# Kernel optimization log

Hardware: AMD Instinct MI355X
Metric: run time of the kernel (lower is better)

## Reference

```python
import jax, jax.numpy as jnp
import numpy as np

L, B, D, H = 2048, 2, 1024, 16
HD = D // H
NEG_INF = float('-inf')


def setup_inputs() -> dict:
    key = jax.random.key(0)
    ks = jax.random.split(key, 12)
    query = jax.random.normal(ks[0], (L, B, D), jnp.float32)
    key_t = jax.random.normal(ks[1], (L, B, D), jnp.float32)
    value = jax.random.normal(ks[2], (L, B, D), jnp.float32)
    # causal attention mask (True = masked)
    attn_mask = jnp.triu(jnp.ones((L, L), dtype=bool), k=1)
    # pad last 128 source positions of batch element 1
    key_pad_mask = jnp.zeros((B, L), dtype=bool).at[1, L - 128:].set(True)
    s = 1.0 / np.sqrt(D)
    Wq = jax.random.normal(ks[3], (D, D), jnp.float32) * s
    bq = jnp.zeros((D,), jnp.float32)
    Wk = jax.random.normal(ks[4], (D, D), jnp.float32) * s
    bk = jnp.zeros((D,), jnp.float32)
    Wv = jax.random.normal(ks[5], (D, D), jnp.float32) * s
    bv = jnp.zeros((D,), jnp.float32)
    Wo = jax.random.normal(ks[6], (D, D), jnp.float32) * s
    bo = jnp.zeros((D,), jnp.float32)
    return {"query": query, "key": key_t, "value": value,
            "key_pad_mask": key_pad_mask, "attn_mask": attn_mask,
            "Wq": Wq, "bq": bq, "Wk": Wk, "bk": bk,
            "Wv": Wv, "bv": bv, "Wo": Wo, "bo": bo}


def reference(query, key, value, key_pad_mask, attn_mask,
              Wq, bq, Wk, bk, Wv, bv, Wo, bo):
    # projections: torch Linear is x @ W.T + b
    q = query @ Wq.T + bq          # (L, B, D)
    k = key @ Wk.T + bk            # (L, B, D)
    v = value @ Wv.T + bv          # (L, B, D)
    # split heads: (L, B, D) -> (B, H, L, hd)
    def split(x):
        return x.reshape(L, B, H, HD).transpose(1, 2, 0, 3)
    q, k, v = split(q), split(k), split(v)
    # NOTE: source module never applies scale_factor (bug kept for fidelity)
    scores = jnp.einsum('bhld,bhsd->bhls', q, k)  # (B, H, L, L)
    scores = jnp.where(attn_mask[None, None, :, :], NEG_INF, scores)
    scores = jnp.where(key_pad_mask[:, None, None, :], NEG_INF, scores)
    attn = jax.nn.softmax(scores, axis=-1)
    # dropout is identity in eval mode
    out = jnp.einsum('bhls,bhsd->bhld', attn, v)  # (B, H, L, hd)
    out = out.transpose(2, 0, 1, 3).reshape(L, B, D)
    return out @ Wo.T + bo
```

## Files before the change

kernel.cpp:

```cpp
#include <hip/hip_runtime.h>
#include <hip/hip_bf16.h>

#define LL 2048
#define BB 2
#define DD 1024
#define HH 16
#define HDIM 64
#define MM (LL*BB)
#define PADROW 30

typedef _Float16 f16x8 __attribute__((ext_vector_type(8)));
typedef _Float16 f16x4 __attribute__((ext_vector_type(4)));
typedef float   f32x4  __attribute__((ext_vector_type(4)));
typedef float   f32x16 __attribute__((ext_vector_type(16)));
typedef unsigned int u32x4 __attribute__((ext_vector_type(4)));

__device__ __forceinline__ void gload16(const void* g, void* l) {
  __builtin_amdgcn_global_load_lds(
      (const __attribute__((address_space(1))) void*)g,
      (__attribute__((address_space(3))) void*)l,
      16, 0, 0);
}

__device__ __forceinline__ unsigned int pkrtz(float a, float b) {
  auto r = __builtin_amdgcn_cvt_pkrtz(a, b);
  return __builtin_bit_cast(unsigned int, r);
}

__global__ __launch_bounds__(256) void cvt_f32_f16(
    const float* __restrict__ q, const float* __restrict__ k, const float* __restrict__ v,
    const float* __restrict__ wq, const float* __restrict__ wk,
    const float* __restrict__ wv, const float* __restrict__ wo,
    _Float16* __restrict__ xq, _Float16* __restrict__ xk, _Float16* __restrict__ xv,
    _Float16* __restrict__ whq, _Float16* __restrict__ whk,
    _Float16* __restrict__ whv, _Float16* __restrict__ who)
{
  const float* s; _Float16* d; int n;
  switch (blockIdx.y) {
    case 0: s = q;  d = xq;  n = MM*DD;  break;
    case 1: s = k;  d = xk;  n = MM*DD;  break;
    case 2: s = v;  d = xv;  n = MM*DD;  break;
    case 3: s = wq; d = whq; n = DD*DD;  break;
    case 4: s = wk; d = whk; n = DD*DD;  break;
    case 5: s = wv; d = whv; n = DD*DD;  break;
    default: s = wo; d = who; n = DD*DD; break;
  }
  int i = (blockIdx.x * 256 + threadIdx.x) * 8;
  if (i >= n) return;
  float4 a = *reinterpret_cast<const float4*>(s + i);
  float4 b = *reinterpret_cast<const float4*>(s + i + 4);
  f16x8 h;
  h[0] = (_Float16)a.x; h[1] = (_Float16)a.y; h[2] = (_Float16)a.z; h[3] = (_Float16)a.w;
  h[4] = (_Float16)b.x; h[5] = (_Float16)b.y; h[6] = (_Float16)b.z; h[7] = (_Float16)b.w;
  *reinterpret_cast<f16x8*>(d + i) = h;
}

__global__ __launch_bounds__(256) void gemm_nt(
    const _Float16* __restrict__ X0, const _Float16* __restrict__ X1, const _Float16* __restrict__ X2,
    const _Float16* __restrict__ W0, const _Float16* __restrict__ W1, const _Float16* __restrict__ W2,
    const float* __restrict__ B0, const float* __restrict__ B1, const float* __restrict__ B2,
    _Float16* __restrict__ dq, _Float16* __restrict__ dk, _Float16* __restrict__ dvt,
    float* __restrict__ dof, int mode_base)
{
  const int K = DD;
  __shared__ alignas(16) _Float16 Ah[128][64];
  __shared__ alignas(16) _Float16 Bh[128][64];
  int z = blockIdx.z;
  const _Float16* X = (z == 0) ? X0 : ((z == 1) ? X1 : X2);
  const _Float16* W = (z == 0) ? W0 : ((z == 1) ? W1 : W2);
  const float* bias = (z == 0) ? B0 : ((z == 1) ? B1 : B2);
  int mode = mode_base + z;
  int tid = threadIdx.x, w = tid >> 6, lane = tid & 63;
  int bb = blockIdx.x;
  int mt = ((bb & 7) * 4 + ((bb >> 3) & 3)) * 128;
  int nt = (bb >> 5) * 128;

  f32x4 acc[4][4];
  #pragma unroll
  for (int i = 0; i < 4; ++i)
    #pragma unroll
    for (int j = 0; j < 4; ++j) acc[i][j] = (f32x4){0.f, 0.f, 0.f, 0.f};

  for (int kt = 0; kt < K; kt += 64) {
    __syncthreads();
    #pragma unroll
    for (int i = 0; i < 4; ++i) {
      int r0 = w * 32 + i * 8;
      int row = r0 + (lane >> 3);
      gload16(X + (size_t)(mt + row) * K + kt + (lane & 7) * 8, &Ah[r0][0]);
      gload16(W + (size_t)(nt + row) * K + kt + (lane & 7) * 8, &Bh[r0][0]);
    }
    __syncthreads();
    #pragma unroll
    for (int kk = 0; kk < 2; ++kk) {
      f16x8 af[4], bf[4];
      #pragma unroll
      for (int f = 0; f < 4; ++f) {
        af[f] = *(const f16x8*)&Ah[(w >> 1) * 64 + f * 16 + (lane & 15)][kk * 32 + (lane >> 4) * 8];
        bf[f] = *(const f16x8*)&Bh[(w & 1) * 64 + f * 16 + (lane & 15)][kk * 32 + (lane >> 4) * 8];
      }
      #pragma unroll
      for (int fm = 0; fm < 4; ++fm)
        #pragma unroll
        for (int fn = 0; fn < 4; ++fn)
          acc[fm][fn] = __builtin_amdgcn_mfma_f32_16x16x32_f16(af[fm], bf[fn], acc[fm][fn], 0, 0, 0);
    }
  }

  #pragma unroll
  for (int fm = 0; fm < 4; ++fm) {
    #pragma unroll
    for (int fn = 0; fn < 4; ++fn) {
      #pragma unroll
      for (int j = 0; j < 4; ++j) {
        int m = mt + (w >> 1) * 64 + fm * 16 + (lane >> 4) * 4 + j;
        int n = nt + (w & 1) * 64 + fn * 16 + (lane & 15);
        float val = acc[fm][fn][j] + bias[n];
        if (mode == 3) {
          dof[(size_t)m * DD + n] = val;
        } else {
          int lseq = m >> 1, bb2 = m & 1;
          int h = n >> 6, hd = n & 63;
          int bh = bb2 * HH + h;
          int s = hd >> 4, hi2 = (hd >> 3) & 1, ii = hd & 7;
          if (mode == 0) {
            int g = lseq >> 5, lo2 = lseq & 31;
            size_t idx = ((((size_t)(bh * 64 + g)) * 4 + s) * 64 + (hi2 * 32 + lo2)) * 8 + ii;
            dq[idx] = (_Float16)val;
          } else if (mode == 1) {
            int t = lseq >> 6, u = (lseq >> 5) & 1, lo2 = lseq & 31;
            size_t idx = ((((size_t)(bh * 32 + t)) * 8 + (u * 4 + s)) * 64 + (hi2 * 32 + lo2)) * 8 + ii;
            dk[idx] = (_Float16)val;
          } else {
            int t = lseq >> 6, rem = lseq & 63;
            int ks = rem >> 4, hiv = (rem >> 3) & 1, iv = rem & 7;
            int vv = hd >> 5, lov = hd & 31;
            size_t idx = ((((size_t)(bh * 32 + t)) * 8 + (vv * 4 + ks)) * 64 + (hiv * 32 + lov)) * 8 + iv;
            dvt[idx] = (_Float16)val;
          }
        }
      }
    }
  }
}

__global__ __launch_bounds__(64, 2) void attn_partial(
    const _Float16* __restrict__ q_ws,
    const _Float16* __restrict__ k_ws,
    const _Float16* __restrict__ vt_ws,
    _Float16* __restrict__ po,
    float* __restrict__ pm,
    float* __restrict__ pl)
{
  int lane = threadIdx.x;
  int lo = lane & 31, hi = lane >> 5;

  int lin = blockIdx.x;
  int k8 = lin & 7, m2 = lin >> 3;
  int half = m2 & 1;
  int bh = k8 * 4 + ((m2 >> 1) & 3);
  int g = 63 - (m2 >> 3);
  int b = bh >> 4;

  const int td = g >> 1;
  int np = td + 1;
  if (b == 1 && np > PADROW) np = PADROW;
  int h1 = (np + 1) >> 1;
  int c0 = half ? h1 : 0;
  int c1 = half ? np : h1;

  int qab = g * 32 + lo;

  f32x16 o0, o1;
  #pragma unroll
  for (int r = 0; r < 16; ++r) { o0[r] = 0.f; o1[r] = 0.f; }
  float m_run = -1e30f, l_run = 0.f;

  if (c0 < c1) {
    const _Float16* qb = q_ws + ((size_t)(bh * 64 + g)) * 2048 + lane * 8;
    f16x8 qf[4];
    #pragma unroll
    for (int s = 0; s < 4; ++s) qf[s] = *(const f16x8*)(qb + s * 512);

    auto loadK = [&](int t, f16x8 (&kf)[8]) __attribute__((always_inline)) {
      const _Float16* kg = k_ws + ((size_t)(bh * 32 + t)) * 4096 + lane * 8;
      #pragma unroll
      for (int f = 0; f < 8; ++f)
        kf[f] = *(const f16x8*)(kg + f * 512);
    };

    auto body = [&](int t, const f16x8 (&kf)[8]) __attribute__((always_inline)) {
      f16x8 vf[8];
      const _Float16* vg = vt_ws + ((size_t)(bh * 32 + t)) * 4096 + lane * 8;
      #pragma unroll
      for (int f = 0; f < 8; ++f)
        vf[f] = *(const f16x8*)(vg + f * 512);

      f32x16 s0, s1;
      #pragma unroll
      for (int r = 0; r < 16; ++r) { s0[r] = 0.f; s1[r] = 0.f; }
      #pragma unroll
      for (int s = 0; s < 4; ++s) {
        s0 = __builtin_amdgcn_mfma_f32_32x32x16_f16(kf[s],     qf[s], s0, 0, 0, 0);
        s1 = __builtin_amdgcn_mfma_f32_32x32x16_f16(kf[4 + s], qf[s], s1, 0, 0, 0);
      }

      if (t == td) {
        #pragma unroll
        for (int r = 0; r < 16; ++r) {
          int kv0 = t * 64 + (r & 3) + 8 * (r >> 2) + 4 * hi;
          if (kv0 > qab)      s0[r] = -1e30f;
          if (kv0 + 32 > qab) s1[r] = -1e30f;
        }
      }

      float pmax = -1e30f;
      #pragma unroll
      for (int r = 0; r < 16; ++r) pmax = fmaxf(pmax, fmaxf(s0[r], s1[r]));
      pmax = fmaxf(pmax, __shfl_xor(pmax, 32));
      float mn = fmaxf(m_run, pmax);
      float sc = __expf(m_run - mn);
      m_run = mn;
      float rs = 0.f;
      #pragma unroll
      for (int r = 0; r < 16; ++r) {
        s0[r] = __expf(s0[r] - mn); rs += s0[r];
        s1[r] = __expf(s1[r] - mn); rs += s1[r];
      }
      rs += __shfl_xor(rs, 32);
      l_run = l_run * sc + rs;
      #pragma unroll
      for (int r = 0; r < 16; ++r) { o0[r] *= sc; o1[r] *= sc; }

      unsigned int W0[8], W1[8];
      #pragma unroll
      for (int wi = 0; wi < 8; ++wi) {
        int r0 = (wi >> 1) * 4 + (wi & 1) * 2;
        W0[wi] = pkrtz(s0[r0], s0[r0 + 1]);
        W1[wi] = pkrtz(s1[r0], s1[r0 + 1]);
      }

      #define DO_KS(W, KS, VA, VB)                                            \
      {                                                                       \
        const int q4 = ((KS) & 1) * 4;                                        \
        unsigned int sA = hi ? W[q4 + 0] : W[q4 + 2];                         \
        unsigned int sB = hi ? W[q4 + 1] : W[q4 + 3];                         \
        unsigned int rA = (unsigned int)__shfl_xor((int)sA, 32);              \
        unsigned int rB = (unsigned int)__shfl_xor((int)sB, 32);              \
        unsigned int own0 = hi ? W[q4 + 2] : W[q4 + 0];                       \
        unsigned int own1 = hi ? W[q4 + 3] : W[q4 + 1];                       \
        u32x4 wv;                                                             \
        wv[0] = hi ? rA : own0;  wv[1] = hi ? rB : own1;                      \
        wv[2] = hi ? own0 : rA;  wv[3] = hi ? own1 : rB;                      \
        f16x8 PB = __builtin_bit_cast(f16x8, wv);                             \
        o0 = __builtin_amdgcn_mfma_f32_32x32x16_f16(VA, PB, o0, 0, 0, 0);     \
        o1 = __builtin_amdgcn_mfma_f32_32x32x16_f16(VB, PB, o1, 0, 0, 0);     \
      }
      DO_KS(W0, 0, vf[0], vf[4])
      DO_KS(W0, 1, vf[1], vf[5])
      DO_KS(W1, 2, vf[2], vf[6])
      DO_KS(W1, 3, vf[3], vf[7])
      #undef DO_KS
    };

    f16x8 kfA[8], kfB[8];
    int t = c0;
    loadK(t, kfA);
    while (true) {
      if (t + 1 < c1) loadK(t + 1, kfB);
      body(t, kfA);
      if (++t >= c1) break;
      if (t + 1 < c1) loadK(t + 1, kfA);
      body(t, kfB);
      if (++t >= c1) break;
    }
  }

  size_t pidx = ((size_t)(bh * 64 + g) << 1) | half;
  _Float16* pb = po + pidx * 2048 + (size_t)lo * 64;
  #pragma unroll
  for (int rq = 0; rq < 4; ++rq) {
    f16x4 a, c;
    #pragma unroll
    for (int j = 0; j < 4; ++j) {
      a[j] = (_Float16)o0[rq * 4 + j];
      c[j] = (_Float16)o1[rq * 4 + j];
    }
    *(f16x4*)(pb + rq * 8 + hi * 4)      = a;
    *(f16x4*)(pb + 32 + rq * 8 + hi * 4) = c;
  }
  if (hi == 0) {
    pm[pidx * 32 + lo] = m_run;
    pl[pidx * 32 + lo] = l_run;
  }
}

__global__ __launch_bounds__(256) void attn_merge(
    const _Float16* __restrict__ po, const float* __restrict__ pm,
    const float* __restrict__ pl, _Float16* __restrict__ ao)
{
  int tid = threadIdx.x;
  int rowl = tid >> 3, dseg = tid & 7;
  int grow = blockIdx.x * 32 + rowl;
  int bh = grow >> 11;
  int rem = grow & 2047;
  int g = rem >> 5;
  int rr = rem & 31;
  size_t pidxA = ((size_t)(bh * 64 + g)) << 1;
  size_t pidxB = pidxA | 1;
  float mA = pm[pidxA * 32 + rr], mB = pm[pidxB * 32 + rr];
  float lA = pl[pidxA * 32 + rr], lB = pl[pidxB * 32 + rr];
  float mx = fmaxf(mA, mB);
  float fA = __expf(mA - mx), fB = __expf(mB - mx);
  float inv = 1.0f / (lA * fA + lB * fB);
  f16x8 a = *(const f16x8*)&po[pidxA * 2048 + rr * 64 + dseg * 8];
  f16x8 bvv = *(const f16x8*)&po[pidxB * 2048 + rr * 64 + dseg * 8];
  f16x8 outv;
  #pragma unroll
  for (int i = 0; i < 8; ++i)
    outv[i] = (_Float16)((((float)a[i]) * fA + ((float)bvv[i]) * fB) * inv);
  int b = bh >> 4, h = bh & 15;
  *(f16x8*)&ao[((size_t)rem * BB + b) * DD + h * 64 + dseg * 8] = outv;
}

extern "C" void kernel_launch(void* const* d_in, const int* in_sizes, int n_in,
                              void* d_out, int out_size, void* d_ws, size_t ws_size,
                              hipStream_t stream) {
  const float* q  = (const float*)d_in[0];
  const float* k  = (const float*)d_in[1];
  const float* v  = (const float*)d_in[2];
  const float* Wq = (const float*)d_in[5];
  const float* bq = (const float*)d_in[6];
  const float* Wk = (const float*)d_in[7];
  const float* bk = (const float*)d_in[8];
  const float* Wv = (const float*)d_in[9];
  const float* bv = (const float*)d_in[10];
  const float* Wo = (const float*)d_in[11];
  const float* bo = (const float*)d_in[12];
  float* out = (float*)d_out;

  _Float16* ws = (_Float16*)d_ws;
  const size_t MD = (size_t)MM * DD;
  const size_t WD = (size_t)DD * DD;
  _Float16* xq   = ws;
  _Float16* xk   = xq + MD;
  _Float16* xv   = xk + MD;
  _Float16* whq  = xv + MD;
  _Float16* whk  = whq + WD;
  _Float16* whv  = whk + WD;
  _Float16* who  = whv + WD;
  _Float16* qws  = who + WD;
  _Float16* kws  = qws + MD;
  _Float16* vtws = kws + MD;
  _Float16* aows = vtws + MD;

  _Float16* po = ws;
  float* pm = (float*)(ws + 3 * MD);
  float* pl = pm + 4096 * 32;

  cvt_f32_f16<<<dim3(2048, 7), 256, 0, stream>>>(
      q, k, v, Wq, Wk, Wv, Wo, xq, xk, xv, whq, whk, whv, who);

  gemm_nt<<<dim3(256, 1, 3), 256, 0, stream>>>(
      xq, xk, xv, whq, whk, whv, bq, bk, bv, qws, kws, vtws, nullptr, 0);

  attn_partial<<<dim3(4096), 64, 0, stream>>>(qws, kws, vtws, po, pm, pl);

  attn_merge<<<dim3(2048), 256, 0, stream>>>(po, pm, pl, aows);

  gemm_nt<<<dim3(256, 1, 1), 256, 0, stream>>>(
      aows, nullptr, nullptr, who, nullptr, nullptr, bo, nullptr, nullptr,
      nullptr, nullptr, nullptr, out, 3);
}
```

Before: 144.7 us.

## Double-buffer GEMM shared-memory tiles to overlap global loads with MFMA

The projection GEMM now keeps two shared buffers and steps K in chunks of 32 instead of 64. The next chunk is issued with async global-to-LDS loads while MFMAs run on the current one, leaving a single barrier per step. This is meant to hide global load latency behind compute. In exchange there are twice as many K iterations and barriers, each doing less MFMA work, and a correctness risk if the async LDS loads are not guaranteed complete by the barrier.

New measurement: 135.4 us. 1.07x faster.

```diff
diff --git a/kernel.cpp b/kernel.cpp
--- a/kernel.cpp
+++ b/kernel.cpp
@@ -63,8 +63,9 @@
     float* __restrict__ dof, int mode_base)
 {
   const int K = DD;
-  __shared__ alignas(16) _Float16 Ah[128][64];
-  __shared__ alignas(16) _Float16 Bh[128][64];
+  const int NSTEP = K / 32;
+  __shared__ alignas(16) _Float16 Ah[2][128][32];
+  __shared__ alignas(16) _Float16 Bh[2][128][32];
   int z = blockIdx.z;
   const _Float16* X = (z == 0) ? X0 : ((z == 1) ? X1 : X2);
   const _Float16* W = (z == 0) ? W0 : ((z == 1) ? W1 : W2);
@@ -75,36 +76,42 @@
   int mt = ((bb & 7) * 4 + ((bb >> 3) & 3)) * 128;
   int nt = (bb >> 5) * 128;
 
+  int srow = w * 32 + (lane >> 2);
+  int scol = (lane & 3) * 8;
+
+  auto stage = [&](int buf, int kt) __attribute__((always_inline)) {
+    gload16(X + (size_t)(mt + srow) * K + kt + scol,      &Ah[buf][w * 32][0]);
+    gload16(X + (size_t)(mt + srow + 16) * K + kt + scol, &Ah[buf][w * 32 + 16][0]);
+    gload16(W + (size_t)(nt + srow) * K + kt + scol,      &Bh[buf][w * 32][0]);
+    gload16(W + (size_t)(nt + srow + 16) * K + kt + scol, &Bh[buf][w * 32 + 16][0]);
+  };
+
   f32x4 acc[4][4];
   #pragma unroll
   for (int i = 0; i < 4; ++i)
     #pragma unroll
     for (int j = 0; j < 4; ++j) acc[i][j] = (f32x4){0.f, 0.f, 0.f, 0.f};
 
-  for (int kt = 0; kt < K; kt += 64) {
+  stage(0, 0);
+  __syncthreads();
+
+  for (int t = 0; t < NSTEP; ++t) {
+    int cur = t & 1;
+    if (t + 1 < NSTEP) stage(cur ^ 1, (t + 1) * 32);
+
+    f16x8 af[4], bf[4];
+    #pragma unroll
+    for (int f = 0; f < 4; ++f) {
+      af[f] = *(const f16x8*)&Ah[cur][(w >> 1) * 64 + f * 16 + (lane & 15)][(lane >> 4) * 8];
+      bf[f] = *(const f16x8*)&Bh[cur][(w & 1) * 64 + f * 16 + (lane & 15)][(lane >> 4) * 8];
+    }
+    #pragma unroll
+    for (int fm = 0; fm < 4; ++fm)
+      #pragma unroll
+      for (int fn = 0; fn < 4; ++fn)
+        acc[fm][fn] = __builtin_amdgcn_mfma_f32_16x16x32_f16(af[fm], bf[fn], acc[fm][fn], 0, 0, 0);
+
     __syncthreads();
-    #pragma unroll
-    for (int i = 0; i < 4; ++i) {
-      int r0 = w * 32 + i * 8;
-      int row = r0 + (lane >> 3);
-      gload16(X + (size_t)(mt + row) * K + kt + (lane & 7) * 8, &Ah[r0][0]);
-      gload16(W + (size_t)(nt + row) * K + kt + (lane & 7) * 8, &Bh[r0][0]);
-    }
-    __syncthreads();
-    #pragma unroll
-    for (int kk = 0; kk < 2; ++kk) {
-      f16x8 af[4], bf[4];
-      #pragma unroll
-      for (int f = 0; f < 4; ++f) {
-        af[f] = *(const f16x8*)&Ah[(w >> 1) * 64 + f * 16 + (lane & 15)][kk * 32 + (lane >> 4) * 8];
-        bf[f] = *(const f16x8*)&Bh[(w & 1) * 64 + f * 16 + (lane & 15)][kk * 32 + (lane >> 4) * 8];
-      }
-      #pragma unroll
-      for (int fm = 0; fm < 4; ++fm)
-        #pragma unroll
-        for (int fn = 0; fn < 4; ++fn)
-          acc[fm][fn] = __builtin_amdgcn_mfma_f32_16x16x32_f16(af[fm], bf[fn], acc[fm][fn], 0, 0, 0);
-    }
   }
 
   #pragma unroll
```

## Pre-swizzle GEMM operands into MFMA fragment layout and drop LDS staging

Applied to the files above, without the earlier changes.

The f32-to-f16 conversion now writes inputs and weights in a fragment-major layout where each 16x32 MFMA fragment is 64 contiguous 16-byte lane chunks, and the attention merge writes its output in the same layout. The GEMM becomes a single-wave 64x64 tile kernel that loads fragments straight from global memory into registers with a double-buffered register pipeline, removing LDS staging and block barriers. The cost is that each operand is reloaded by many more small blocks, with no LDS reuse across waves, so it relies on L2 hits; the conversion kernel also adds an LDS transpose step.

After: 132.5 us. 8.4% less time.

```diff
diff --git a/kernel.cpp b/kernel.cpp
--- a/kernel.cpp
+++ b/kernel.cpp
@@ -15,19 +15,13 @@
 typedef float   f32x16 __attribute__((ext_vector_type(16)));
 typedef unsigned int u32x4 __attribute__((ext_vector_type(4)));
 
-__device__ __forceinline__ void gload16(const void* g, void* l) {
-  __builtin_amdgcn_global_load_lds(
-      (const __attribute__((address_space(1))) void*)g,
-      (__attribute__((address_space(3))) void*)l,
-      16, 0, 0);
-}
-
 __device__ __forceinline__ unsigned int pkrtz(float a, float b) {
   auto r = __builtin_amdgcn_cvt_pkrtz(a, b);
   return __builtin_bit_cast(unsigned int, r);
 }
 
-__global__ __launch_bounds__(256) void cvt_f32_f16(
+
+__global__ __launch_bounds__(256) void cvt_frag(
     const float* __restrict__ q, const float* __restrict__ k, const float* __restrict__ v,
     const float* __restrict__ wq, const float* __restrict__ wk,
     const float* __restrict__ wv, const float* __restrict__ wo,
@@ -35,45 +29,77 @@
     _Float16* __restrict__ whq, _Float16* __restrict__ whk,
     _Float16* __restrict__ whv, _Float16* __restrict__ who)
 {
-  const float* s; _Float16* d; int n;
+  __shared__ alignas(16) _Float16 lds[16][264];
+  const float* s; _Float16* d; int R;
   switch (blockIdx.y) {
-    case 0: s = q;  d = xq;  n = MM*DD;  break;
-    case 1: s = k;  d = xk;  n = MM*DD;  break;
-    case 2: s = v;  d = xv;  n = MM*DD;  break;
-    case 3: s = wq; d = whq; n = DD*DD;  break;
-    case 4: s = wk; d = whk; n = DD*DD;  break;
-    case 5: s = wv; d = whv; n = DD*DD;  break;
-    default: s = wo; d = who; n = DD*DD; break;
-  }
-  int i = (blockIdx.x * 256 + threadIdx.x) * 8;
-  if (i >= n) return;
-  float4 a = *reinterpret_cast<const float4*>(s + i);
-  float4 b = *reinterpret_cast<const float4*>(s + i + 4);
-  f16x8 h;
-  h[0] = (_Float16)a.x; h[1] = (_Float16)a.y; h[2] = (_Float16)a.z; h[3] = (_Float16)a.w;
-  h[4] = (_Float16)b.x; h[5] = (_Float16)b.y; h[6] = (_Float16)b.z; h[7] = (_Float16)b.w;
-  *reinterpret_cast<f16x8*>(d + i) = h;
-}
-
-__global__ __launch_bounds__(256) void gemm_nt(
+    case 0: s = q;  d = xq;  R = MM;  break;
+    case 1: s = k;  d = xk;  R = MM;  break;
+    case 2: s = v;  d = xv;  R = MM;  break;
+    case 3: s = wq; d = whq; R = DD;  break;
+    case 4: s = wk; d = whk; R = DD;  break;
+    case 5: s = wv; d = whv; R = DD;  break;
+    default: s = wo; d = who; R = DD; break;
+  }
+  int bi = blockIdx.x;
+  if (bi >= (R >> 4) * 4) return;
+  int g = bi >> 2, q4 = bi & 3;
+  int kc0 = q4 * 256;
+  int t = threadIdx.x;
+
+  int rr = t >> 6, cc = (t & 63) * 4;
+  #pragma unroll
+  for (int rep = 0; rep < 4; ++rep) {
+    int row = rep * 4 + rr;
+    float4 vv = *reinterpret_cast<const float4*>(s + (size_t)(g * 16 + row) * DD + kc0 + cc);
+    lds[row][cc]     = (_Float16)vv.x;
+    lds[row][cc + 1] = (_Float16)vv.y;
+    lds[row][cc + 2] = (_Float16)vv.z;
+    lds[row][cc + 3] = (_Float16)vv.w;
+  }
+  __syncthreads();
+
+  #pragma unroll
+  for (int rep = 0; rep < 2; ++rep) {
+    int slot = rep * 256 + t;
+    int cell = slot >> 6, lane2 = slot & 63;
+    int r2 = lane2 & 15, k2 = cell * 32 + (lane2 >> 4) * 8;
+    f16x8 h;
+    #pragma unroll
+    for (int i = 0; i < 8; ++i) h[i] = lds[r2][k2 + i];
+    size_t gcell = (size_t)g * 32 + q4 * 8 + cell;
+    *(f16x8*)(d + (gcell * 64 + lane2) * 8) = h;
+  }
+}
+
+__global__ __launch_bounds__(64, 2) void gemm_frag(
     const _Float16* __restrict__ X0, const _Float16* __restrict__ X1, const _Float16* __restrict__ X2,
     const _Float16* __restrict__ W0, const _Float16* __restrict__ W1, const _Float16* __restrict__ W2,
     const float* __restrict__ B0, const float* __restrict__ B1, const float* __restrict__ B2,
     _Float16* __restrict__ dq, _Float16* __restrict__ dk, _Float16* __restrict__ dvt,
     float* __restrict__ dof, int mode_base)
 {
-  const int K = DD;
-  __shared__ alignas(16) _Float16 Ah[128][64];
-  __shared__ alignas(16) _Float16 Bh[128][64];
+  const int NSTEP = DD / 32;
+  int lane = threadIdx.x;
   int z = blockIdx.z;
   const _Float16* X = (z == 0) ? X0 : ((z == 1) ? X1 : X2);
   const _Float16* W = (z == 0) ? W0 : ((z == 1) ? W1 : W2);
   const float* bias = (z == 0) ? B0 : ((z == 1) ? B1 : B2);
   int mode = mode_base + z;
-  int tid = threadIdx.x, w = tid >> 6, lane = tid & 63;
-  int bb = blockIdx.x;
-  int mt = ((bb & 7) * 4 + ((bb >> 3) & 3)) * 128;
-  int nt = (bb >> 5) * 128;
+
+  int lin = blockIdx.x;
+  int xcd = lin & 7, inner = lin >> 3;
+  int mtile = xcd * 8 + (inner >> 4);
+  int ntile = inner & 15;
+
+  const _Float16* pa = X + (size_t)(mtile * 4) * 16384 + lane * 8;
+  const _Float16* pb = W + (size_t)(ntile * 4) * 16384 + lane * 8;
+
+  auto loadF = [&](int s, f16x8 (&af)[4], f16x8 (&bf)[4]) __attribute__((always_inline)) {
+    #pragma unroll
+    for (int i = 0; i < 4; ++i) af[i] = *(const f16x8*)(pa + i * 16384 + s * 512);
+    #pragma unroll
+    for (int i = 0; i < 4; ++i) bf[i] = *(const f16x8*)(pb + i * 16384 + s * 512);
+  };
 
   f32x4 acc[4][4];
   #pragma unroll
@@ -81,40 +107,35 @@
     #pragma unroll
     for (int j = 0; j < 4; ++j) acc[i][j] = (f32x4){0.f, 0.f, 0.f, 0.f};
 
-  for (int kt = 0; kt < K; kt += 64) {
-    __syncthreads();
-    #pragma unroll
-    for (int i = 0; i < 4; ++i) {
-      int r0 = w * 32 + i * 8;
-      int row = r0 + (lane >> 3);
-      gload16(X + (size_t)(mt + row) * K + kt + (lane & 7) * 8, &Ah[r0][0]);
-      gload16(W + (size_t)(nt + row) * K + kt + (lane & 7) * 8, &Bh[r0][0]);
-    }
-    __syncthreads();
-    #pragma unroll
-    for (int kk = 0; kk < 2; ++kk) {
-      f16x8 af[4], bf[4];
-      #pragma unroll
-      for (int f = 0; f < 4; ++f) {
-        af[f] = *(const f16x8*)&Ah[(w >> 1) * 64 + f * 16 + (lane & 15)][kk * 32 + (lane >> 4) * 8];
-        bf[f] = *(const f16x8*)&Bh[(w & 1) * 64 + f * 16 + (lane & 15)][kk * 32 + (lane >> 4) * 8];
-      }
-      #pragma unroll
-      for (int fm = 0; fm < 4; ++fm)
-        #pragma unroll
-        for (int fn = 0; fn < 4; ++fn)
-          acc[fm][fn] = __builtin_amdgcn_mfma_f32_16x16x32_f16(af[fm], bf[fn], acc[fm][fn], 0, 0, 0);
-    }
-  }
-
+  auto domfma = [&](const f16x8 (&af)[4], const f16x8 (&bf)[4]) __attribute__((always_inline)) {
+    #pragma unroll
+    for (int fm = 0; fm < 4; ++fm)
+      #pragma unroll
+      for (int fn = 0; fn < 4; ++fn)
+        acc[fm][fn] = __builtin_amdgcn_mfma_f32_16x16x32_f16(af[fm], bf[fn], acc[fm][fn], 0, 0, 0);
+  };
+
+  f16x8 aA[4], bA[4], aB[4], bB[4];
+  loadF(0, aA, bA);
+  int s = 0;
+  while (true) {
+    if (s + 1 < NSTEP) loadF(s + 1, aB, bB);
+    domfma(aA, bA);
+    if (++s >= NSTEP) break;
+    if (s + 1 < NSTEP) loadF(s + 1, aA, bA);
+    domfma(aB, bB);
+    if (++s >= NSTEP) break;
+  }
+
+  int mt = mtile * 64, nt = ntile * 64;
   #pragma unroll
   for (int fm = 0; fm < 4; ++fm) {
     #pragma unroll
     for (int fn = 0; fn < 4; ++fn) {
       #pragma unroll
       for (int j = 0; j < 4; ++j) {
-        int m = mt + (w >> 1) * 64 + fm * 16 + (lane >> 4) * 4 + j;
-        int n = nt + (w & 1) * 64 + fn * 16 + (lane & 15);
+        int m = mt + fm * 16 + (lane >> 4) * 4 + j;
+        int n = nt + fn * 16 + (lane & 15);
         float val = acc[fm][fn][j] + bias[n];
         if (mode == 3) {
           dof[(size_t)m * DD + n] = val;
@@ -122,14 +143,14 @@
           int lseq = m >> 1, bb2 = m & 1;
           int h = n >> 6, hd = n & 63;
           int bh = bb2 * HH + h;
-          int s = hd >> 4, hi2 = (hd >> 3) & 1, ii = hd & 7;
+          int sx = hd >> 4, hi2 = (hd >> 3) & 1, ii = hd & 7;
           if (mode == 0) {
             int g = lseq >> 5, lo2 = lseq & 31;
-            size_t idx = ((((size_t)(bh * 64 + g)) * 4 + s) * 64 + (hi2 * 32 + lo2)) * 8 + ii;
+            size_t idx = ((((size_t)(bh * 64 + g)) * 4 + sx) * 64 + (hi2 * 32 + lo2)) * 8 + ii;
             dq[idx] = (_Float16)val;
           } else if (mode == 1) {
             int t = lseq >> 6, u = (lseq >> 5) & 1, lo2 = lseq & 31;
-            size_t idx = ((((size_t)(bh * 32 + t)) * 8 + (u * 4 + s)) * 64 + (hi2 * 32 + lo2)) * 8 + ii;
+            size_t idx = ((((size_t)(bh * 32 + t)) * 8 + (u * 4 + sx)) * 64 + (hi2 * 32 + lo2)) * 8 + ii;
             dk[idx] = (_Float16)val;
           } else {
             int t = lseq >> 6, rem = lseq & 63;
@@ -320,7 +341,11 @@
   for (int i = 0; i < 8; ++i)
     outv[i] = (_Float16)((((float)a[i]) * fA + ((float)bvv[i]) * fB) * inv);
   int b = bh >> 4, h = bh & 15;
-  *(f16x8*)&ao[((size_t)rem * BB + b) * DD + h * 64 + dseg * 8] = outv;
+  int m = rem * BB + b;
+  int kk = h * 64 + dseg * 8;
+  size_t gcell = (size_t)(m >> 4) * 32 + (kk >> 5);
+  int lane2 = (m & 15) | (((kk >> 3) & 3) << 4);
+  *(f16x8*)&ao[(gcell * 64 + lane2) * 8] = outv;
 }
 
 extern "C" void kernel_launch(void* const* d_in, const int* in_sizes, int n_in,
@@ -358,17 +383,17 @@
   float* pm = (float*)(ws + 3 * MD);
   float* pl = pm + 4096 * 32;
 
-  cvt_f32_f16<<<dim3(2048, 7), 256, 0, stream>>>(
+  cvt_frag<<<dim3(1024, 7), 256, 0, stream>>>(
       q, k, v, Wq, Wk, Wv, Wo, xq, xk, xv, whq, whk, whv, who);
 
-  gemm_nt<<<dim3(256, 1, 3), 256, 0, stream>>>(
+  gemm_frag<<<dim3(1024, 1, 3), 64, 0, stream>>>(
       xq, xk, xv, whq, whk, whv, bq, bk, bv, qws, kws, vtws, nullptr, 0);
 
   attn_partial<<<dim3(4096), 64, 0, stream>>>(qws, kws, vtws, po, pm, pl);
 
   attn_merge<<<dim3(2048), 256, 0, stream>>>(po, pm, pl, aows);
 
-  gemm_nt<<<dim3(256, 1, 1), 256, 0, stream>>>(
+  gemm_frag<<<dim3(1024, 1, 1), 64, 0, stream>>>(
       aows, nullptr, nullptr, who, nullptr, nullptr, bo, nullptr, nullptr,
       nullptr, nullptr, nullptr, out, 3);
 }
```
